# Kernel tuning notes

Hardware: AMD Instinct MI355X
Metric: run time of the kernel (lower is better)

Reference implementation:

```python
import jax, jax.numpy as jnp
import numpy as np

N, D, K = 131072, 512, 1024


def setup_inputs() -> dict:
    key = jax.random.key(0)
    k1, k2 = jax.random.split(key)
    features = jax.random.normal(k1, (N, D), dtype=jnp.float32)
    centroids = jax.random.normal(k2, (D, K), dtype=jnp.float32)
    return {"features": features, "centroids": centroids}


def reference(features, centroids):
    # Squared Euclidean distance via norm expansion (avoids [N, D, K] broadcast):
    x_sq = jnp.sum(features * features, axis=1, keepdims=True)      # [N, 1]
    c_sq = jnp.sum(centroids * centroids, axis=0, keepdims=True)    # [1, K]
    cross = jnp.einsum('nd,dk->nk', features, centroids)            # [N, K]
    distances = x_sq - 2.0 * cross + c_sq                           # [N, K]
    assignments = jnp.argmin(distances, axis=-1)                    # [N]
    return assignments[:, None].astype(jnp.float32)                 # [N, 1]
```

## Files before the change

kernel.cpp:

```cpp
#include <hip/hip_runtime.h>
#include <hip/hip_bf16.h>

#define NPTS 131072
#define DIMS 512
#define KC   1024

typedef _Float16 f16;
using f16x8  = __attribute__((ext_vector_type(8))) _Float16;
using f32x16 = __attribute__((ext_vector_type(16))) float;
typedef unsigned short u16;
typedef unsigned int u32;
typedef unsigned long long u64;

#define CT_OFF     0ull
#define CSQ_OFF    1048576ull
#define CSQP_OFF   1052672ull
#define G1_OFF     1118208ull
#define G2_OFF     2166784ull
#define CNT_OFF    3215360ull
#define LIST_OFF   3215616ull
#define WS_NEEDED  3739904ull

#define MARGIN 0.2f

__device__ __forceinline__ u32 f2o(float f) {
    u32 u = __float_as_uint(f);
    return (u & 0x80000000u) ? ~u : (u | 0x80000000u);
}
__device__ __forceinline__ float o2f(u32 o) {
    u32 u = (o & 0x80000000u) ? (o & 0x7FFFFFFFu) : ~o;
    return __uint_as_float(u);
}
__device__ __forceinline__ u64 umin64(u64 a, u64 b) { return a < b ? a : b; }
__device__ __forceinline__ u64 umax64(u64 a, u64 b) { return a > b ? a : b; }

__device__ __forceinline__ void async_load16(const void* g, const void* l) {
    auto gp = reinterpret_cast<__attribute__((address_space(1))) void*>(
        reinterpret_cast<uintptr_t>(g));
    auto lp = reinterpret_cast<__attribute__((address_space(3))) void*>(
        (unsigned int)reinterpret_cast<uintptr_t>(l));
    __builtin_amdgcn_global_load_lds(gp, lp, 16, 0, 0);
}

__global__ void split_c_kernel(const float* __restrict__ C,
                               u16* __restrict__ ct, float* __restrict__ csq_part) {
    __shared__ float t[32][33];
    int bn = blockIdx.x, bd = blockIdx.y;
    int tx = threadIdx.x & 31, ty = threadIdx.x >> 5;
#pragma unroll
    for (int r = 0; r < 32; r += 8)
        t[ty + r][tx] = C[(size_t)(bd * 32 + ty + r) * KC + bn * 32 + tx];
    __syncthreads();
#pragma unroll
    for (int r = 0; r < 32; r += 8) {
        int n = bn * 32 + ty + r, d = bd * 32 + tx;
        float v = t[tx][ty + r];
        f16 h = (f16)v;
        ct[(size_t)n * DIMS + d] = *reinterpret_cast<u16*>(&h);
        float sq = v * v;
#pragma unroll
        for (int m = 1; m < 32; m <<= 1)
            sq += __shfl_xor(sq, m, 64);
        if (tx == 0) csq_part[bd * KC + n] = sq;
    }
}

__global__ void csq_reduce_kernel(const float* __restrict__ part, float* __restrict__ csq) {
    int k = blockIdx.x * 256 + threadIdx.x;
    float s = 0.f;
#pragma unroll
    for (int p = 0; p < 16; ++p) s += part[p * KC + k];
    csq[k] = s;
}

__global__ void csq_kernel(const float* __restrict__ C, float* __restrict__ csq) {
    int k = blockIdx.x * blockDim.x + threadIdx.x;
    if (k < KC) {
        float s = 0.f;
        for (int d = 0; d < DIMS; ++d) {
            float v = C[d * KC + k];
            s = fmaf(v, v, s);
        }
        csq[k] = s;
    }
}

__global__ __launch_bounds__(256, 4) void gemm_argmin_kernel(
    const float* __restrict__ F, const u16* __restrict__ Ct,
    const float* __restrict__ csq, u64* __restrict__ g1, u64* __restrict__ g2)
{
    __shared__ __align__(16) uint8_t smem[16384];

    const int tid  = threadIdx.x;
    const int lane = tid & 63;
    const int wid  = tid >> 6;
    const int wm   = wid >> 1, wn = wid & 1;
    const unsigned L = blockIdx.x;
    const int by = (int)((L & 7u) + 8u * (L >> 6));
    const int bx = (int)((L >> 3) & 7u);

    f32x16 acc[2][2];
#pragma unroll
    for (int i = 0; i < 2; ++i)
#pragma unroll
        for (int j = 0; j < 2; ++j)
#pragma unroll
            for (int e = 0; e < 16; ++e) acc[i][j][e] = 0.f;

    const int arow = tid >> 1, ah_ = tid & 1;
    const float* aF = F + (size_t)(by * 128 + arow) * DIMS + ah_ * 16;
    const int axr = (arow >> 1) & 3;
    const unsigned aw0 = (unsigned)(arow * 64 + (((ah_ * 2 + 0) ^ axr) * 16));
    const unsigned aw1 = (unsigned)(arow * 64 + (((ah_ * 2 + 1) ^ axr) * 16));

    const int c_st = (lane & 3) ^ ((lane >> 3) & 3);
    const u16* bBase = Ct + (size_t)(bx * 128 + wid * 32 + (lane >> 2)) * DIMS + c_st * 8;
    const unsigned bw = 8192 + (unsigned)(wid * 32) * 64;

    const int kh = lane >> 5;
    const int cl = lane & 31;
    const int xr = (cl >> 1) & 3;
    const unsigned mb = (unsigned)cl * 64;
    const unsigned offs0 = mb + (unsigned)(((0 + kh) ^ xr) * 16);
    const unsigned offs1 = mb + (unsigned)(((2 + kh) ^ xr) * 16);

    for (int kt = 0; kt < DIMS / 32; ++kt) {
        const int k0 = kt * 32;
        float4 f0 = *(const float4*)(aF + k0);
        float4 f1 = *(const float4*)(aF + k0 + 4);
        float4 f2 = *(const float4*)(aF + k0 + 8);
        float4 f3 = *(const float4*)(aF + k0 + 12);

        __syncthreads();
        async_load16(bBase + k0,            smem + bw);
        async_load16(bBase + 16 * DIMS + k0, smem + bw + 1024);
        {
            float v[16] = {f0.x, f0.y, f0.z, f0.w, f1.x, f1.y, f1.z, f1.w,
                           f2.x, f2.y, f2.z, f2.w, f3.x, f3.y, f3.z, f3.w};
            f16x8 h0, h1;
#pragma unroll
            for (int i = 0; i < 8; ++i) h0[i] = (f16)v[i];
#pragma unroll
            for (int i = 0; i < 8; ++i) h1[i] = (f16)v[8 + i];
            *(f16x8*)(smem + aw0) = h0;
            *(f16x8*)(smem + aw1) = h1;
        }
        __syncthreads();

#pragma unroll
        for (int s = 0; s < 2; ++s) {
            const unsigned off = s ? offs1 : offs0;
            f16x8 a[2], b[2];
#pragma unroll
            for (int mt = 0; mt < 2; ++mt)
                a[mt] = *(const f16x8*)(smem + wm * 4096 + mt * 2048 + off);
#pragma unroll
            for (int nt = 0; nt < 2; ++nt)
                b[nt] = *(const f16x8*)(smem + 8192 + wn * 4096 + nt * 2048 + off);
#pragma unroll
            for (int mt = 0; mt < 2; ++mt)
#pragma unroll
                for (int nt = 0; nt < 2; ++nt)
                    acc[mt][nt] = __builtin_amdgcn_mfma_f32_32x32x16_f16(a[mt], b[nt], acc[mt][nt], 0, 0, 0);
        }
    }

    __syncthreads();
    u64* tbl = (u64*)smem;

    const int colbase = bx * 128 + wn * 64 + cl;
    const float cs0 = csq[colbase], cs1 = csq[colbase + 32];

#pragma unroll
    for (int mt = 0; mt < 2; ++mt)
#pragma unroll
        for (int reg = 0; reg < 16; ++reg) {
            const int row = wm * 64 + mt * 32 + (reg & 3) + 8 * (reg >> 2) + 4 * kh;
            float d0 = cs0 - 2.0f * acc[mt][0][reg];
            float d1 = cs1 - 2.0f * acc[mt][1][reg];
            u64 k0 = ((u64)f2o(d0) << 32) | (u32)colbase;
            u64 k1 = ((u64)f2o(d1) << 32) | (u32)(colbase + 32);
            u64 a = umin64(k0, k1), b = umax64(k0, k1);
#pragma unroll
            for (int off = 16; off > 0; off >>= 1) {
                u64 oa = __shfl_xor(a, off, 64);
                u64 ob = __shfl_xor(b, off, 64);
                u64 lo = umin64(a, oa), hi = umax64(a, oa);
                b = umin64(hi, umin64(b, ob));
                a = lo;
            }
            if (cl == 0) { tbl[(row * 2 + wn) * 2] = a; tbl[(row * 2 + wn) * 2 + 1] = b; }
        }
    __syncthreads();

    if (tid < 128) {
        const u64 a0 = tbl[tid * 4 + 0], b0 = tbl[tid * 4 + 1];
        const u64 a1 = tbl[tid * 4 + 2], b1 = tbl[tid * 4 + 3];
        u64 m1 = umin64(a0, a1);
        u64 m2 = umin64(umax64(a0, a1), umin64(b0, b1));
        const size_t grow = (size_t)by * 128 + tid;
        u64 o = atomicMin(&g1[grow], m1);
        atomicMin(&g2[grow], (m1 < o) ? o : m1);
        atomicMin(&g2[grow], m2);
    }
}

__global__ __launch_bounds__(256) void flag_compact_kernel(
    const u64* __restrict__ g1, const u64* __restrict__ g2,
    float* __restrict__ out, u32* __restrict__ cnt, u32* __restrict__ list)
{
    __shared__ u32 lcnt, lbase;
    __shared__ u32 lrows[256];
    const int tid = threadIdx.x;
    const int row = blockIdx.x * 256 + tid;
    if (tid == 0) lcnt = 0;
    __syncthreads();

    const u64 k1 = g1[row], k2 = g2[row];
    const float d1 = o2f((u32)(k1 >> 32));
    const float d2 = o2f((u32)(k2 >> 32));
    bool flagged = !(d2 - d1 > MARGIN);
    if (!flagged) {
        out[row] = (float)(u32)(k1 & 1023u);
    } else {
        u32 li = atomicAdd(&lcnt, 1u);
        lrows[li] = (u32)row;
    }
    __syncthreads();
    if (tid == 0 && lcnt > 0) lbase = atomicAdd(cnt, lcnt);
    __syncthreads();
    if (tid < lcnt) list[lbase + tid] = lrows[tid];
}

__global__ __launch_bounds__(256) void rescue2_kernel(
    const float* __restrict__ F, const float* __restrict__ C,
    const float* __restrict__ csq, const u32* __restrict__ cnt,
    const u32* __restrict__ list, u32* __restrict__ wptr, float* __restrict__ out)
{
    __shared__ float xs[4][512];
    __shared__ u64 wavemin[4][4];
    __shared__ int rows_s[4];

    const int tid = threadIdx.x;
    const int lane = tid & 63;
    const int wid = tid >> 6;
    const u32 n = cnt[0];

    for (;;) {
        __syncthreads();
        u32 base;
        if (tid == 0) {
            base = atomicAdd(wptr, 4u);
            rows_s[0] = (int)base;
        }
        __syncthreads();
        base = (u32)rows_s[0];
        if (base >= n) break;

        int rows[4];
#pragma unroll
        for (int j = 0; j < 4; ++j) {
            u32 idx = base + j;
            rows[j] = (int)list[idx < n ? idx : (n - 1)];
        }
#pragma unroll
        for (int j = 0; j < 4; ++j) {
            if (tid < 128)
                *(float4*)&xs[j][tid * 4] = *(const float4*)&F[(size_t)rows[j] * DIMS + tid * 4];
        }
        __syncthreads();

        float dot[4][4];
#pragma unroll
        for (int j = 0; j < 4; ++j)
#pragma unroll
            for (int q = 0; q < 4; ++q) dot[j][q] = 0.f;

#pragma unroll 4
        for (int d = 0; d < DIMS; ++d) {
            float cv[4];
#pragma unroll
            for (int q = 0; q < 4; ++q) cv[q] = C[d * KC + tid + 256 * q];
            float xv[4];
#pragma unroll
            for (int j = 0; j < 4; ++j) xv[j] = xs[j][d];
#pragma unroll
            for (int j = 0; j < 4; ++j)
#pragma unroll
                for (int q = 0; q < 4; ++q)
                    dot[j][q] = fmaf(xv[j], cv[q], dot[j][q]);
        }

#pragma unroll
        for (int j = 0; j < 4; ++j) {
            u64 best = ~0ull;
#pragma unroll
            for (int q = 0; q < 4; ++q) {
                const int k = tid + 256 * q;
                const float dist = csq[k] - 2.0f * dot[j][q];
                best = umin64(best, ((u64)f2o(dist) << 32) | (u32)k);
            }
#pragma unroll
            for (int off = 32; off > 0; off >>= 1)
                best = umin64(best, __shfl_xor(best, off, 64));
            if (lane == 0) wavemin[j][wid] = best;
        }
        __syncthreads();
        if (tid < 4) {
            const u32 idx = base + tid;
            if (idx < n) {
                u64 b = umin64(umin64(wavemin[tid][0], wavemin[tid][1]),
                               umin64(wavemin[tid][2], wavemin[tid][3]));
                out[list[idx]] = (float)(u32)(b & 0xFFFFFFFFull);
            }
        }
    }
}

__global__ __launch_bounds__(256, 3) void assign_kernel_fp32(
    const float* __restrict__ F, const float* __restrict__ C,
    const float* __restrict__ csq, float* __restrict__ out)
{
    __shared__ float At[32][68];
    __shared__ float Bs[32 * 256];
    __shared__ u64 best_row[64];

    const int tid = threadIdx.x;
    const int tx = tid & 31;
    const int ty = tid >> 5;
    const int n0 = blockIdx.x * 64;

    if (tid < 64) best_row[tid] = ~0ull;

    u64 best[8];
#pragma unroll
    for (int r = 0; r < 8; ++r) best[r] = ~0ull;

    const int arow = tid >> 3;
    const int ac4  = tid & 7;
    const float* Atp = &At[0][ty * 8];
    const float* Bsp = &Bs[tx * 4];

    for (int kt = 0; kt < 4; ++kt) {
        float acc[8][8];
#pragma unroll
        for (int r = 0; r < 8; ++r)
#pragma unroll
            for (int j = 0; j < 8; ++j) acc[r][j] = 0.f;

        for (int dt = 0; dt < DIMS / 32; ++dt) {
            __syncthreads();
#pragma unroll
            for (int i = 0; i < 2; ++i) {
                int row = arow + 32 * i;
                float4 av = *(const float4*)&F[(long)(n0 + row) * DIMS + dt * 32 + ac4 * 4];
                At[ac4 * 4 + 0][row] = av.x;
                At[ac4 * 4 + 1][row] = av.y;
                At[ac4 * 4 + 2][row] = av.z;
                At[ac4 * 4 + 3][row] = av.w;
            }
#pragma unroll
            for (int i = 0; i < 8; ++i) {
                int idx = tid + 256 * i;
                int d  = idx >> 6;
                int c4 = idx & 63;
                float4 bv = *(const float4*)&C[(long)(dt * 32 + d) * KC + kt * 256 + c4 * 4];
                *(float4*)&Bs[d * 256 + c4 * 4] = bv;
            }
            __syncthreads();

#pragma unroll 8
            for (int dd = 0; dd < 32; ++dd) {
                float4 a0 = *(const float4*)(Atp + dd * 68);
                float4 a1 = *(const float4*)(Atp + dd * 68 + 4);
                float4 b0 = *(const float4*)(Bsp + dd * 256);
                float4 b1 = *(const float4*)(Bsp + dd * 256 + 128);
                float a[8] = {a0.x, a0.y, a0.z, a0.w, a1.x, a1.y, a1.z, a1.w};
                float bb[8] = {b0.x, b0.y, b0.z, b0.w, b1.x, b1.y, b1.z, b1.w};
#pragma unroll
                for (int r = 0; r < 8; ++r)
#pragma unroll
                    for (int j = 0; j < 8; ++j)
                        acc[r][j] = fmaf(a[r], bb[j], acc[r][j]);
            }
        }

        float4 cs0 = *(const float4*)&csq[kt * 256 + tx * 4];
        float4 cs1 = *(const float4*)&csq[kt * 256 + 128 + tx * 4];
        float cs[8] = {cs0.x, cs0.y, cs0.z, cs0.w, cs1.x, cs1.y, cs1.z, cs1.w};
#pragma unroll
        for (int j = 0; j < 8; ++j) {
            int k = kt * 256 + ((j < 4) ? (tx * 4 + j) : (128 + tx * 4 + (j - 4)));
#pragma unroll
            for (int r = 0; r < 8; ++r) {
                float val = cs[j] - 2.0f * acc[r][j];
                u64 key = ((u64)f2o(val) << 32) | (u64)(unsigned)k;
                if (key < best[r]) best[r] = key;
            }
        }
    }

#pragma unroll
    for (int r = 0; r < 8; ++r)
        atomicMin(&best_row[ty * 8 + r], best[r]);
    __syncthreads();

    if (tid < 64)
        out[n0 + tid] = (float)(unsigned)(best_row[tid] & 0xFFFFFFFFull);
}

extern "C" void kernel_launch(void* const* d_in, const int* in_sizes, int n_in,
                              void* d_out, int out_size, void* d_ws, size_t ws_size,
                              hipStream_t stream) {
    const float* F = (const float*)d_in[0];
    const float* C = (const float*)d_in[1];
    float* out = (float*)d_out;
    char* ws = (char*)d_ws;

    if (ws_size < WS_NEEDED) {
        float* csq = (float*)d_ws;
        csq_kernel<<<KC / 256, 256, 0, stream>>>(C, csq);
        assign_kernel_fp32<<<NPTS / 64, 256, 0, stream>>>(F, C, csq, out);
        return;
    }

    u16* Ct = (u16*)(ws + CT_OFF);
    float* csq  = (float*)(ws + CSQ_OFF);
    float* csqp = (float*)(ws + CSQP_OFF);
    u64* g1 = (u64*)(ws + G1_OFF);
    u64* g2 = (u64*)(ws + G2_OFF);
    u32* cnt  = (u32*)(ws + CNT_OFF);
    u32* list = (u32*)(ws + LIST_OFF);

    hipMemsetAsync(g1, 0xFF, 2ull * NPTS * 8, stream);
    hipMemsetAsync(cnt, 0, 8, stream);
    split_c_kernel<<<dim3(KC / 32, DIMS / 32), 256, 0, stream>>>(C, Ct, csqp);
    csq_reduce_kernel<<<KC / 256, 256, 0, stream>>>(csqp, csq);
    gemm_argmin_kernel<<<8192, 256, 0, stream>>>(F, Ct, csq, g1, g2);
    flag_compact_kernel<<<NPTS / 256, 256, 0, stream>>>(g1, g2, out, cnt, list);
    rescue2_kernel<<<1024, 256, 0, stream>>>(F, C, csq, cnt, list, cnt + 1, out);
}
```

Before: 766.2 us.

## Swap GEMM operand roles so argmin reduces within lanes instead of shuffles

Centroids now feed the MFMA A operand (rows of the tile) and points feed the B operand, so each lane holds many centroid distances for one point. The top-2 argmin over centroids becomes an in-register scan per lane followed by a single cross-half shuffle, replacing the five-step 64-bit shuffle butterfly that ran for every output register. Centroid norms are staged in shared memory and indexed per row. The cost is a different shared-memory tile mapping and per-register LDS reads of the centroid norms.

```diff
diff --git a/kernel.cpp b/kernel.cpp
--- a/kernel.cpp
+++ b/kernel.cpp
@@ -90,14 +90,17 @@
     const float* __restrict__ csq, u64* __restrict__ g1, u64* __restrict__ g2)
 {
     __shared__ __align__(16) uint8_t smem[16384];
+    __shared__ float csq_l[128];
 
     const int tid  = threadIdx.x;
     const int lane = tid & 63;
     const int wid  = tid >> 6;
     const int wm   = wid >> 1, wn = wid & 1;
     const unsigned L = blockIdx.x;
-    const int by = (int)((L & 7u) + 8u * (L >> 6));
-    const int bx = (int)((L >> 3) & 7u);
+    const int py = (int)((L & 7u) + 8u * (L >> 6));
+    const int cx = (int)((L >> 3) & 7u);
+
+    if (tid < 128) csq_l[tid] = csq[cx * 128 + tid];
 
     f32x16 acc[2][2];
 #pragma unroll
@@ -107,15 +110,15 @@
 #pragma unroll
             for (int e = 0; e < 16; ++e) acc[i][j][e] = 0.f;
 
-    const int arow = tid >> 1, ah_ = tid & 1;
-    const float* aF = F + (size_t)(by * 128 + arow) * DIMS + ah_ * 16;
-    const int axr = (arow >> 1) & 3;
-    const unsigned aw0 = (unsigned)(arow * 64 + (((ah_ * 2 + 0) ^ axr) * 16));
-    const unsigned aw1 = (unsigned)(arow * 64 + (((ah_ * 2 + 1) ^ axr) * 16));
+    const int brow = tid >> 1, bh_ = tid & 1;
+    const float* bF = F + (size_t)(py * 128 + brow) * DIMS + bh_ * 16;
+    const int bxr = (brow >> 1) & 3;
+    const unsigned bw0 = 8192u + (unsigned)(brow * 64 + (((bh_ * 2 + 0) ^ bxr) * 16));
+    const unsigned bw1 = 8192u + (unsigned)(brow * 64 + (((bh_ * 2 + 1) ^ bxr) * 16));
 
     const int c_st = (lane & 3) ^ ((lane >> 3) & 3);
-    const u16* bBase = Ct + (size_t)(bx * 128 + wid * 32 + (lane >> 2)) * DIMS + c_st * 8;
-    const unsigned bw = 8192 + (unsigned)(wid * 32) * 64;
+    const u16* aBase = Ct + (size_t)(cx * 128 + wid * 32 + (lane >> 2)) * DIMS + c_st * 8;
+    const unsigned aw = (unsigned)(wid * 32) * 64;
 
     const int kh = lane >> 5;
     const int cl = lane & 31;
@@ -126,14 +129,14 @@
 
     for (int kt = 0; kt < DIMS / 32; ++kt) {
         const int k0 = kt * 32;
-        float4 f0 = *(const float4*)(aF + k0);
-        float4 f1 = *(const float4*)(aF + k0 + 4);
-        float4 f2 = *(const float4*)(aF + k0 + 8);
-        float4 f3 = *(const float4*)(aF + k0 + 12);
-
-        __syncthreads();
-        async_load16(bBase + k0,            smem + bw);
-        async_load16(bBase + 16 * DIMS + k0, smem + bw + 1024);
+        float4 f0 = *(const float4*)(bF + k0);
+        float4 f1 = *(const float4*)(bF + k0 + 4);
+        float4 f2 = *(const float4*)(bF + k0 + 8);
+        float4 f3 = *(const float4*)(bF + k0 + 12);
+
+        __syncthreads();
+        async_load16(aBase + k0,             smem + aw);
+        async_load16(aBase + 16 * DIMS + k0, smem + aw + 1024);
         {
             float v[16] = {f0.x, f0.y, f0.z, f0.w, f1.x, f1.y, f1.z, f1.w,
                            f2.x, f2.y, f2.z, f2.w, f3.x, f3.y, f3.z, f3.w};
@@ -142,8 +145,8 @@
             for (int i = 0; i < 8; ++i) h0[i] = (f16)v[i];
 #pragma unroll
             for (int i = 0; i < 8; ++i) h1[i] = (f16)v[8 + i];
-            *(f16x8*)(smem + aw0) = h0;
-            *(f16x8*)(smem + aw1) = h1;
+            *(f16x8*)(smem + bw0) = h0;
+            *(f16x8*)(smem + bw1) = h1;
         }
         __syncthreads();
 
@@ -168,29 +171,30 @@
     __syncthreads();
     u64* tbl = (u64*)smem;
 
-    const int colbase = bx * 128 + wn * 64 + cl;
-    const float cs0 = csq[colbase], cs1 = csq[colbase + 32];
-
-#pragma unroll
-    for (int mt = 0; mt < 2; ++mt)
-#pragma unroll
-        for (int reg = 0; reg < 16; ++reg) {
-            const int row = wm * 64 + mt * 32 + (reg & 3) + 8 * (reg >> 2) + 4 * kh;
-            float d0 = cs0 - 2.0f * acc[mt][0][reg];
-            float d1 = cs1 - 2.0f * acc[mt][1][reg];
-            u64 k0 = ((u64)f2o(d0) << 32) | (u32)colbase;
-            u64 k1 = ((u64)f2o(d1) << 32) | (u32)(colbase + 32);
-            u64 a = umin64(k0, k1), b = umax64(k0, k1);
-#pragma unroll
-            for (int off = 16; off > 0; off >>= 1) {
-                u64 oa = __shfl_xor(a, off, 64);
-                u64 ob = __shfl_xor(b, off, 64);
-                u64 lo = umin64(a, oa), hi = umax64(a, oa);
-                b = umin64(hi, umin64(b, ob));
-                a = lo;
-            }
-            if (cl == 0) { tbl[(row * 2 + wn) * 2] = a; tbl[(row * 2 + wn) * 2 + 1] = b; }
-        }
+#pragma unroll
+    for (int nt = 0; nt < 2; ++nt) {
+        u64 a = ~0ull, b = ~0ull;
+#pragma unroll
+        for (int mt = 0; mt < 2; ++mt)
+#pragma unroll
+            for (int reg = 0; reg < 16; ++reg) {
+                const int rl = wm * 64 + mt * 32 + (reg & 3) + 8 * (reg >> 2) + 4 * kh;
+                const float d = fmaf(-2.0f, acc[mt][nt][reg], csq_l[rl]);
+                const u64 key = ((u64)f2o(d) << 32) | (u32)(cx * 128 + rl);
+                const u64 t = umin64(a, key);
+                b = umin64(b, umax64(a, key));
+                a = t;
+            }
+        const u64 oa = __shfl_xor(a, 32, 64);
+        const u64 ob = __shfl_xor(b, 32, 64);
+        const u64 lo = umin64(a, oa);
+        const u64 bb = umin64(umax64(a, oa), umin64(b, ob));
+        if (kh == 0) {
+            const int p = wn * 64 + nt * 32 + cl;
+            tbl[(p * 2 + wm) * 2 + 0] = lo;
+            tbl[(p * 2 + wm) * 2 + 1] = bb;
+        }
+    }
     __syncthreads();
 
     if (tid < 128) {
@@ -198,7 +202,7 @@
         const u64 a1 = tbl[tid * 4 + 2], b1 = tbl[tid * 4 + 3];
         u64 m1 = umin64(a0, a1);
         u64 m2 = umin64(umax64(a0, a1), umin64(b0, b1));
-        const size_t grow = (size_t)by * 128 + tid;
+        const size_t grow = (size_t)py * 128 + tid;
         u64 o = atomicMin(&g1[grow], m1);
         atomicMin(&g2[grow], (m1 < o) ? o : m1);
         atomicMin(&g2[grow], m2);
```

Result: slower. 949.4 us (+23.9%).
